# Kernel tuning notes

Hardware: AMD Instinct MI355X
Metric: run time of the kernel (lower is better)

## Reference

```python
import jax, jax.numpy as jnp
import numpy as np

B, N, D = 4096, 64, 128
H = 2
M = 3 * D            # model_dim = feat + edge + time
DK = M // H          # d_k = d_v = 192


def setup_inputs() -> dict:
    key = jax.random.key(0)
    ks = jax.random.split(key, 20)
    s = 0.02
    mask = jax.random.randint(ks[6], (B, N), 0, 2).astype(bool)
    mask = mask.at[:, 0].set(False)  # guarantee >=1 valid neighbor per row
    return {
        "src":   jax.random.normal(ks[0], (B, D), jnp.float32),
        "src_t": jax.random.normal(ks[1], (B, 1, D), jnp.float32),
        "src_s": jax.random.normal(ks[2], (B, D), jnp.float32),
        "seq":   jax.random.normal(ks[3], (B, N, D), jnp.float32),
        "seq_t": jax.random.normal(ks[4], (B, N, D), jnp.float32),
        "seq_e": jax.random.normal(ks[5], (B, N, D), jnp.float32),
        "mask":  mask,
        # MapBasedMultiHeadAttention params (torch Linear convention: [out, in])
        "Wq": jax.random.normal(ks[7], (M, M), jnp.float32) * s,
        "Wk": jax.random.normal(ks[8], (M, M), jnp.float32) * s,
        "Wv": jax.random.normal(ks[9], (M, M), jnp.float32) * s,
        "w_map": jax.random.normal(ks[10], (2 * DK,), jnp.float32) * s,
        "Wfc": jax.random.normal(ks[11], (M, M), jnp.float32) * s,
        "bfc": jnp.zeros((M,), jnp.float32),
        "ln_g": jnp.ones((M,), jnp.float32),
        "ln_b": jnp.zeros((M,), jnp.float32),
        # MergeLayer params
        "W1": jax.random.normal(ks[12], (D, M + D), jnp.float32) * s,
        "b1": jnp.zeros((D,), jnp.float32),
        "W2": jax.random.normal(ks[13], (D, D), jnp.float32) * s,
        "b2": jnp.zeros((D,), jnp.float32),
    }


def reference(src, src_t, src_s, seq, seq_t, seq_e, mask,
              Wq, Wk, Wv, w_map, Wfc, bfc, ln_g, ln_b, W1, b1, W2, b2):
    # AttnModel.forward with attn_mode='map', dropout in eval mode.
    q_in = jnp.concatenate([src[:, None, :], src_s[:, None, :], src_t], axis=2)  # [B,1,M]
    k_in = jnp.concatenate([seq, seq_e, seq_t], axis=2)                           # [B,N,M]

    qp = (q_in @ Wq.T).reshape(B, 1, H, DK)   # [B,1,H,dk]
    kp = (k_in @ Wk.T).reshape(B, N, H, DK)   # [B,N,H,dk]
    vp = (k_in @ Wv.T).reshape(B, N, H, DK)   # [B,N,H,dv]

    # weight_map(cat([q,k])) decomposes exactly: w1.q + w2.k (no bias, no nonlinearity before softmax)
    w1, w2 = w_map[:DK], w_map[DK:]
    logit = (jnp.einsum('bqhd,d->bhq', qp, w1)[:, :, :, None]
             + jnp.einsum('bnhd,d->bhn', kp, w2)[:, :, None, :])  # [B,H,1,N]
    logit = jnp.where(mask[:, None, None, :], -1e10, logit)
    attn = jax.nn.softmax(logit, axis=-1)                          # [B,H,1,N]

    out = jnp.einsum('bhqn,bnhd->bqhd', attn, vp).reshape(B, M)    # len_q == 1
    out = jax.nn.leaky_relu(out @ Wfc.T + bfc, negative_slope=0.2)
    out = out + q_in[:, 0, :]                                       # residual
    mu = out.mean(-1, keepdims=True)
    var = ((out - mu) ** 2).mean(-1, keepdims=True)
    out = (out - mu) / jnp.sqrt(var + 1e-5) * ln_g + ln_b           # LayerNorm

    # MergeLayer(output, src)
    x = jnp.concatenate([out, src], axis=1)                         # [B, M+D]
    h = jax.nn.relu(x @ W1.T + b1)
    output = h @ W2.T + b2                                          # [B, D]

    # torch attn after squeeze: [n_head*B, N], head-major
    attn_out = attn[:, :, 0, :].transpose(1, 0, 2).reshape(H * B, N)
    return output, attn_out
```

## Files before the change

### kernel.cpp

```cpp
#include <hip/hip_runtime.h>
#include <hip/hip_bf16.h>

#define B_ 4096
#define N_ 64
#define D_ 128
#define H_ 2
#define M_ 384
#define DK_ 192

#define WS_WKEFF 64
#define WS_W1T   1024
#define WS_W2T   66560
#define WS_WVB   82944
#define WS_WFCB  156672
#define WS_CTXB  230400
#define WS_R     2589696
#define WS_TOTAL 4162560

typedef __attribute__((ext_vector_type(8))) short bf16x8;
typedef __attribute__((ext_vector_type(4))) float f32x4;

__device__ __forceinline__ unsigned short bf1(float a) {
    return __builtin_bit_cast(unsigned short, __float2bfloat16(a));
}

__global__ __launch_bounds__(256) void prep2(
    const float* __restrict__ Wk, const float* __restrict__ wmap,
    const float* __restrict__ W1, const float* __restrict__ W2,
    const float* __restrict__ Wv, const float* __restrict__ Wfc,
    const void* __restrict__ mask, int* __restrict__ flag,
    float* __restrict__ wkeff, float* __restrict__ W1t, float* __restrict__ W2t,
    unsigned short* __restrict__ Wvb, unsigned short* __restrict__ Wfcb) {
    const int tid = threadIdx.x;
    if (blockIdx.x == 0 && tid == 0) {
        const unsigned int* u = (const unsigned int*)mask;
        bool all01 = true, allf = true;
        for (int i = 0; i < 64; ++i) {
            unsigned int v = u[i];
            if (v != 0u && v != 1u) all01 = false;
            if (v != 0u && v != 0x3f800000u) allf = false;
        }
        *flag = all01 ? 0 : (allf ? 2 : 1);
    }
    const int lane = tid & 63, wave = tid >> 6;
    const int gw = blockIdx.x * 4 + wave;
    if (gw < H_ * M_) {
        const int h = gw / M_, m = gw - h * M_;
        float s = 0.f;
        #pragma unroll
        for (int i = 0; i < 3; ++i) {
            int d = lane + i * 64;
            s += wmap[DK_ + d] * Wk[(size_t)(h * DK_ + d) * M_ + m];
        }
        #pragma unroll
        for (int off = 1; off < 64; off <<= 1) s += __shfl_xor(s, off, 64);
        if (lane == 0) wkeff[gw] = s;
    }
    const int gt = blockIdx.x * 256 + tid;
    const int stride = gridDim.x * 256;
    for (int i = gt; i < (M_ + D_) * D_; i += stride) {
        int k = i >> 7, o = i & 127;
        W1t[i] = W1[(size_t)o * (M_ + D_) + k];
    }
    for (int i = gt; i < D_ * D_; i += stride) {
        int k = i >> 7, o = i & 127;
        W2t[i] = W2[(size_t)o * D_ + k];
    }
    for (int i = gt; i < M_ * M_; i += stride) {
        Wvb[i]  = bf1(Wv[i]);
        Wfcb[i] = bf1(Wfc[i]);
    }
}

template <bool NT>
__device__ __forceinline__ float4 ld4(const float* p) {
    if (NT) {
        f32x4 r = __builtin_nontemporal_load((const f32x4*)p);
        return *(float4*)&r;
    }
    return *(const float4*)p;
}

template <bool NT>
__global__ __launch_bounds__(256) void attn_v4k(
    const float* __restrict__ seq, const float* __restrict__ seqE,
    const float* __restrict__ seqT, const void* __restrict__ mask,
    const float* __restrict__ wkeff, const int* __restrict__ flagp,
    unsigned short* __restrict__ ctxb, float* __restrict__ attn_out, int b0off) {
    __shared__ float scacc[4][16][50];
    __shared__ float swl[2][64];
    __shared__ float sel[4][2];

    const int b = blockIdx.x + b0off;
    const int tid = threadIdx.x;
    const int lane = tid & 63;
    const int wv = tid >> 6;
    const int j8 = tid & 15;
    const int g = tid >> 4;
    const int flag = *flagp;

    float wr0[24], wr1[24];
    #pragma unroll
    for (int t = 0; t < 3; ++t) {
        float4 a0 = *(const float4*)&wkeff[t * 128 + j8 * 8];
        float4 a1 = *(const float4*)&wkeff[t * 128 + j8 * 8 + 4];
        float4 b0 = *(const float4*)&wkeff[M_ + t * 128 + j8 * 8];
        float4 b1 = *(const float4*)&wkeff[M_ + t * 128 + j8 * 8 + 4];
        wr0[t*8+0]=a0.x; wr0[t*8+1]=a0.y; wr0[t*8+2]=a0.z; wr0[t*8+3]=a0.w;
        wr0[t*8+4]=a1.x; wr0[t*8+5]=a1.y; wr0[t*8+6]=a1.z; wr0[t*8+7]=a1.w;
        wr1[t*8+0]=b0.x; wr1[t*8+1]=b0.y; wr1[t*8+2]=b0.z; wr1[t*8+3]=b0.w;
        wr1[t*8+4]=b1.x; wr1[t*8+5]=b1.y; wr1[t*8+6]=b1.z; wr1[t*8+7]=b1.w;
    }

    float cacc0[24], cacc1[24];
    #pragma unroll
    for (int j = 0; j < 24; ++j) { cacc0[j] = 0.f; cacc1[j] = 0.f; }
    float el0 = 0.f, el1 = 0.f;

    const size_t bbase = (size_t)b * (N_ * D_);

    #pragma unroll
    for (int it = 0; it < 4; ++it) {
        const int n = g + (it << 4);
        const size_t off = bbase + (size_t)n * 128 + j8 * 8;
        float v[24];
        {
            float4 va0 = ld4<NT>(&seq [off]);
            float4 va1 = ld4<NT>(&seq [off + 4]);
            float4 vb0 = ld4<NT>(&seqE[off]);
            float4 vb1 = ld4<NT>(&seqE[off + 4]);
            float4 vc0 = ld4<NT>(&seqT[off]);
            float4 vc1 = ld4<NT>(&seqT[off + 4]);
            v[0]=va0.x; v[1]=va0.y; v[2]=va0.z; v[3]=va0.w;
            v[4]=va1.x; v[5]=va1.y; v[6]=va1.z; v[7]=va1.w;
            v[8]=vb0.x; v[9]=vb0.y; v[10]=vb0.z; v[11]=vb0.w;
            v[12]=vb1.x; v[13]=vb1.y; v[14]=vb1.z; v[15]=vb1.w;
            v[16]=vc0.x; v[17]=vc0.y; v[18]=vc0.z; v[19]=vc0.w;
            v[20]=vc1.x; v[21]=vc1.y; v[22]=vc1.z; v[23]=vc1.w;
        }
        float a0 = 0.f, a1 = 0.f;
        #pragma unroll
        for (int j = 0; j < 24; ++j) { a0 += v[j] * wr0[j]; a1 += v[j] * wr1[j]; }
        #pragma unroll
        for (int o = 1; o < 16; o <<= 1) {
            a0 += __shfl_xor(a0, o, 64);
            a1 += __shfl_xor(a1, o, 64);
        }
        int mv;
        if (flag == 0)      mv = ((const int*)mask)[(size_t)b * N_ + n];
        else if (flag == 1) mv = ((const unsigned char*)mask)[(size_t)b * N_ + n];
        else                mv = (((const unsigned int*)mask)[(size_t)b * N_ + n] != 0u) ? 1 : 0;
        float w0, w1;
        if (mv) { w0 = 0.f; w1 = 0.f; }
        else    { w0 = __expf(a0); w1 = __expf(a1); }
        el0 += w0; el1 += w1;
        if (j8 == 0) { swl[0][n] = w0; swl[1][n] = w1; }
        #pragma unroll
        for (int j = 0; j < 24; ++j) { cacc0[j] += w0 * v[j]; cacc1[j] += w1 * v[j]; }
    }

    #pragma unroll
    for (int o = 16; o <= 32; o <<= 1) {
        #pragma unroll
        for (int j = 0; j < 24; ++j) {
            cacc0[j] += __shfl_xor(cacc0[j], o, 64);
            cacc1[j] += __shfl_xor(cacc1[j], o, 64);
        }
    }
    #pragma unroll
    for (int o = 1; o < 64; o <<= 1) {
        el0 += __shfl_xor(el0, o, 64);
        el1 += __shfl_xor(el1, o, 64);
    }
    if (lane < 16) {
        float* dst = &scacc[wv][lane][0];
        #pragma unroll
        for (int j = 0; j < 24; ++j) { dst[j] = cacc0[j]; dst[24 + j] = cacc1[j]; }
    }
    if (lane == 0) { sel[wv][0] = el0; sel[wv][1] = el1; }
    __syncthreads();

    const float l0 = (sel[0][0] + sel[1][0] + sel[2][0] + sel[3][0]) * 0.0625f;
    const float l1 = (sel[0][1] + sel[1][1] + sel[2][1] + sel[3][1]) * 0.0625f;
    const float r0i = 1.f / l0, r1i = 1.f / l1;

    for (int o = tid; o < H_ * M_; o += 256) {
        const int h = (o >= M_) ? 1 : 0;
        const int m = o - h * M_;
        const int t = m >> 7, c = m & 127;
        const int jm = c >> 3, jj = c & 7;
        const int idx = h * 24 + t * 8 + jj;
        float s = scacc[0][jm][idx] + scacc[1][jm][idx] + scacc[2][jm][idx] + scacc[3][jm][idx];
        ctxb[(size_t)b * (H_ * M_) + o] = bf1(s * (h ? r1i : r0i));
    }
    if (tid < H_ * N_) {
        const int h = tid >> 6, n = tid & 63;
        attn_out[((size_t)h * B_ + b) * N_ + n] = swl[h][n] * (h ? r1i : r0i);
    }
}

#define SOUTSTRIDE 392
__global__ __launch_bounds__(256) void gemm_vfc(
    const unsigned short* __restrict__ ctxb, const unsigned short* __restrict__ Wvb,
    const unsigned short* __restrict__ Wfcb, const float* __restrict__ bfc,
    const float* __restrict__ src, const float* __restrict__ src_s, const float* __restrict__ src_t,
    float* __restrict__ rws) {
    __shared__ __hip_bfloat16 sout[16 * SOUTSTRIDE];
    const int tid = threadIdx.x;
    const int wave = tid >> 6, lane = tid & 63;
    const int r0 = blockIdx.x * 16;
    const int lr = lane & 15, lk = (lane >> 4) * 8;
    const int aOff = (wave >= 2) ? M_ : 0;

    f32x4 acc[6] = {};
    const unsigned short* arow = &ctxb[(size_t)(r0 + lr) * (H_ * M_) + aOff + lk];
    #pragma unroll
    for (int kk = 0; kk < M_; kk += 32) {
        bf16x8 af = *(const bf16x8*)&arow[kk];
        #pragma unroll
        for (int jt = 0; jt < 6; ++jt) {
            const int j0 = wave * 96 + jt * 16;
            bf16x8 bfr = *(const bf16x8*)&Wvb[(size_t)(j0 + lr) * M_ + kk + lk];
            acc[jt] = __builtin_amdgcn_mfma_f32_16x16x32_bf16(af, bfr, acc[jt], 0, 0, 0);
        }
    }
    #pragma unroll
    for (int jt = 0; jt < 6; ++jt)
        #pragma unroll
        for (int q = 0; q < 4; ++q) {
            const int row = (lane >> 4) * 4 + q;
            sout[row * SOUTSTRIDE + wave * 96 + jt * 16 + lr] =
                __float2bfloat16(acc[jt][q]);
        }
    __syncthreads();

    f32x4 acc2[6] = {};
    #pragma unroll
    for (int kk = 0; kk < M_; kk += 32) {
        bf16x8 af = *(const bf16x8*)&sout[lr * SOUTSTRIDE + kk + lk];
        #pragma unroll
        for (int jt = 0; jt < 6; ++jt) {
            const int j0 = wave * 96 + jt * 16;
            bf16x8 bfr = *(const bf16x8*)&Wfcb[(size_t)(j0 + lr) * M_ + kk + lk];
            acc2[jt] = __builtin_amdgcn_mfma_f32_16x16x32_bf16(af, bfr, acc2[jt], 0, 0, 0);
        }
    }
    #pragma unroll
    for (int jt = 0; jt < 6; ++jt) {
        const int j0 = wave * 96 + jt * 16;
        const float* qsrc = (j0 < D_) ? src : (j0 < 2 * D_) ? src_s : src_t;
        const int joff = j0 - ((j0 < D_) ? 0 : (j0 < 2 * D_) ? D_ : 2 * D_);
        #pragma unroll
        for (int q = 0; q < 4; ++q) {
            const int row = r0 + (lane >> 4) * 4 + q;
            const int jc = j0 + lr;
            float t = acc2[jt][q] + bfc[jc];
            t = t > 0.f ? t : 0.2f * t;
            t += qsrc[(size_t)row * D_ + joff + lr];
            rws[(size_t)row * M_ + jc] = t;
        }
    }
}

__global__ __launch_bounds__(256) void ln_mlp(
    const float* __restrict__ rin, const float* __restrict__ src,
    const float* __restrict__ g, const float* __restrict__ bta,
    const float* __restrict__ W1t, const float* __restrict__ b1,
    const float* __restrict__ W2t, const float* __restrict__ b2,
    float* __restrict__ outp) {
    __shared__ float sa[8 * 520];
    __shared__ float sh[8 * 132];
    const int b0 = blockIdx.x * 8;
    const int tid = threadIdx.x;
    const int row = tid >> 5, part = tid & 31;
    const size_t gr = (size_t)(b0 + row);
    {
        const float* rr = &rin[gr * M_];
        float4 v[3];
        float s = 0.f, sq = 0.f;
        #pragma unroll
        for (int i = 0; i < 3; ++i) {
            v[i] = *(const float4*)&rr[(part + i * 32) * 4];
            s  += v[i].x + v[i].y + v[i].z + v[i].w;
            sq += v[i].x * v[i].x + v[i].y * v[i].y + v[i].z * v[i].z + v[i].w * v[i].w;
        }
        #pragma unroll
        for (int off = 1; off < 32; off <<= 1) {
            s += __shfl_xor(s, off, 64); sq += __shfl_xor(sq, off, 64);
        }
        float mu = s * (1.f / 384.f);
        float rs = rsqrtf(sq * (1.f / 384.f) - mu * mu + 1e-5f);
        #pragma unroll
        for (int i = 0; i < 3; ++i) {
            int k = (part + i * 32) * 4;
            float4 g4 = *(const float4*)&g[k];
            float4 b4 = *(const float4*)&bta[k];
            float4 z;
            z.x = (v[i].x - mu) * rs * g4.x + b4.x;
            z.y = (v[i].y - mu) * rs * g4.y + b4.y;
            z.z = (v[i].z - mu) * rs * g4.z + b4.z;
            z.w = (v[i].w - mu) * rs * g4.w + b4.w;
            *(float4*)&sa[row * 520 + k] = z;
        }
        *(float4*)&sa[row * 520 + M_ + part * 4] = *(const float4*)&src[gr * D_ + part * 4];
    }
    __syncthreads();
    const int c4 = part * 4;
    float acc[4] = {};
    const float* ar = &sa[row * 520];
    #pragma unroll 4
    for (int k4 = 0; k4 < 128; ++k4) {
        float4 a4 = *(const float4*)&ar[k4 * 4];
        #pragma unroll
        for (int j = 0; j < 4; ++j) {
            int k = k4 * 4 + j;
            float a = (j == 0) ? a4.x : (j == 1) ? a4.y : (j == 2) ? a4.z : a4.w;
            float4 w = *(const float4*)&W1t[k * D_ + c4];
            acc[0] += a * w.x; acc[1] += a * w.y; acc[2] += a * w.z; acc[3] += a * w.w;
        }
    }
    {
        float4 bb = *(const float4*)&b1[c4];
        float4 hh;
        hh.x = fmaxf(acc[0] + bb.x, 0.f);
        hh.y = fmaxf(acc[1] + bb.y, 0.f);
        hh.z = fmaxf(acc[2] + bb.z, 0.f);
        hh.w = fmaxf(acc[3] + bb.w, 0.f);
        *(float4*)&sh[row * 132 + c4] = hh;
    }
    __syncthreads();
    float acc2[4] = {};
    const float* hr = &sh[row * 132];
    #pragma unroll 4
    for (int k4 = 0; k4 < 32; ++k4) {
        float4 a4 = *(const float4*)&hr[k4 * 4];
        #pragma unroll
        for (int j = 0; j < 4; ++j) {
            int k = k4 * 4 + j;
            float a = (j == 0) ? a4.x : (j == 1) ? a4.y : (j == 2) ? a4.z : a4.w;
            float4 w = *(const float4*)&W2t[k * D_ + c4];
            acc2[0] += a * w.x; acc2[1] += a * w.y; acc2[2] += a * w.z; acc2[3] += a * w.w;
        }
    }
    float4 bb2 = *(const float4*)&b2[c4];
    float4 oo = make_float4(acc2[0] + bb2.x, acc2[1] + bb2.y, acc2[2] + bb2.z, acc2[3] + bb2.w);
    *(float4*)&outp[gr * D_ + c4] = oo;
}

extern "C" void kernel_launch(void* const* d_in, const int* in_sizes, int n_in,
                              void* d_out, int out_size, void* d_ws, size_t ws_size,
                              hipStream_t stream) {
    (void)in_sizes; (void)n_in; (void)out_size;
    const float* src   = (const float*)d_in[0];
    const float* src_t = (const float*)d_in[1];
    const float* src_s = (const float*)d_in[2];
    const float* seq   = (const float*)d_in[3];
    const float* seq_t = (const float*)d_in[4];
    const float* seq_e = (const float*)d_in[5];
    const void*  mask  = d_in[6];
    const float* Wk    = (const float*)d_in[8];
    const float* Wv    = (const float*)d_in[9];
    const float* wmap  = (const float*)d_in[10];
    const float* Wfc   = (const float*)d_in[11];
    const float* bfc   = (const float*)d_in[12];
    const float* ln_g  = (const float*)d_in[13];
    const float* ln_b  = (const float*)d_in[14];
    const float* W1    = (const float*)d_in[15];
    const float* b1    = (const float*)d_in[16];
    const float* W2    = (const float*)d_in[17];
    const float* b2    = (const float*)d_in[18];

    if (ws_size < (size_t)WS_TOTAL * sizeof(float)) return;
    float* wsf   = (float*)d_ws;
    int*   flagp = (int*)d_ws;
    float* wkeff = wsf + WS_WKEFF;
    float* W1t   = wsf + WS_W1T;
    float* W2t   = wsf + WS_W2T;
    unsigned short* Wvb   = (unsigned short*)(wsf + WS_WVB);
    unsigned short* Wfcb  = (unsigned short*)(wsf + WS_WFCB);
    unsigned short* ctxb  = (unsigned short*)(wsf + WS_CTXB);
    float* rws   = wsf + WS_R;
    float* outp     = (float*)d_out;
    float* attn_out = outp + (size_t)B_ * D_;

    prep2<<<256, 256, 0, stream>>>(Wk, wmap, W1, W2, Wv, Wfc, mask, flagp,
                                   wkeff, W1t, W2t, Wvb, Wfcb);
    attn_v4k<true><<<B_ / 2, 256, 0, stream>>>(seq, seq_e, seq_t, mask, wkeff, flagp,
                                               ctxb, attn_out, 0);
    attn_v4k<false><<<B_ / 2, 256, 0, stream>>>(seq, seq_e, seq_t, mask, wkeff, flagp,
                                                ctxb, attn_out, B_ / 2);
    gemm_vfc<<<256, 256, 0, stream>>>(ctxb, Wvb, Wfcb, bfc, src, src_s, src_t, rws);
    ln_mlp<<<512, 256, 0, stream>>>(rws, src, ln_g, ln_b, W1t, b1, W2t, b2, outp);
}
```

Before: 154.1 us.

## Fuse V/FC GEMM with LayerNorm+MLP and drop nontemporal loads

Merges the bf16 MFMA V/FC GEMM kernel with the LayerNorm and merge-MLP kernel into one 512-thread kernel. The residual rows stay in shared memory instead of round-tripping through a global workspace, which also removes one launch. The attention kernel's nontemporal-load template is replaced by plain loads for both halves. In exchange, the fused kernel runs only 256 blocks for the MLP stage, where the old ln_mlp launched 512, and uses more shared memory per block.

```diff
diff --git a/kernel.cpp b/kernel.cpp
--- a/kernel.cpp
+++ b/kernel.cpp
@@ -14,8 +14,7 @@
 #define WS_WVB   82944
 #define WS_WFCB  156672
 #define WS_CTXB  230400
-#define WS_R     2589696
-#define WS_TOTAL 4162560
+#define WS_TOTAL 1017088
 
 typedef __attribute__((ext_vector_type(8))) short bf16x8;
 typedef __attribute__((ext_vector_type(4))) float f32x4;
@@ -72,17 +71,7 @@
     }
 }
 
-template <bool NT>
-__device__ __forceinline__ float4 ld4(const float* p) {
-    if (NT) {
-        f32x4 r = __builtin_nontemporal_load((const f32x4*)p);
-        return *(float4*)&r;
-    }
-    return *(const float4*)p;
-}
-
-template <bool NT>
-__global__ __launch_bounds__(256) void attn_v4k(
+__global__ __launch_bounds__(256) void attn_v4(
     const float* __restrict__ seq, const float* __restrict__ seqE,
     const float* __restrict__ seqT, const void* __restrict__ mask,
     const float* __restrict__ wkeff, const int* __restrict__ flagp,
@@ -125,12 +114,12 @@
         const size_t off = bbase + (size_t)n * 128 + j8 * 8;
         float v[24];
         {
-            float4 va0 = ld4<NT>(&seq [off]);
-            float4 va1 = ld4<NT>(&seq [off + 4]);
-            float4 vb0 = ld4<NT>(&seqE[off]);
-            float4 vb1 = ld4<NT>(&seqE[off + 4]);
-            float4 vc0 = ld4<NT>(&seqT[off]);
-            float4 vc1 = ld4<NT>(&seqT[off + 4]);
+            float4 va0 = *(const float4*)&seq [off];
+            float4 va1 = *(const float4*)&seq [off + 4];
+            float4 vb0 = *(const float4*)&seqE[off];
+            float4 vb1 = *(const float4*)&seqE[off + 4];
+            float4 vc0 = *(const float4*)&seqT[off];
+            float4 vc1 = *(const float4*)&seqT[off + 4];
             v[0]=va0.x; v[1]=va0.y; v[2]=va0.z; v[3]=va0.w;
             v[4]=va1.x; v[5]=va1.y; v[6]=va1.z; v[7]=va1.w;
             v[8]=vb0.x; v[9]=vb0.y; v[10]=vb0.z; v[11]=vb0.w;
@@ -200,87 +189,84 @@
 }
 
 #define SOUTSTRIDE 392
-__global__ __launch_bounds__(256) void gemm_vfc(
+__global__ __launch_bounds__(512) void gemm_vfc_ln(
     const unsigned short* __restrict__ ctxb, const unsigned short* __restrict__ Wvb,
     const unsigned short* __restrict__ Wfcb, const float* __restrict__ bfc,
     const float* __restrict__ src, const float* __restrict__ src_s, const float* __restrict__ src_t,
-    float* __restrict__ rws) {
+    const float* __restrict__ g, const float* __restrict__ bta,
+    const float* __restrict__ W1t, const float* __restrict__ b1,
+    const float* __restrict__ W2t, const float* __restrict__ b2,
+    float* __restrict__ outp) {
     __shared__ __hip_bfloat16 sout[16 * SOUTSTRIDE];
+    __shared__ float sa[16 * 520];
+    __shared__ float sh[16 * 132];
     const int tid = threadIdx.x;
     const int wave = tid >> 6, lane = tid & 63;
     const int r0 = blockIdx.x * 16;
     const int lr = lane & 15, lk = (lane >> 4) * 8;
-    const int aOff = (wave >= 2) ? M_ : 0;
-
-    f32x4 acc[6] = {};
+    const int aOff = (wave >= 4) ? M_ : 0;
+
+    f32x4 acc[3] = {};
     const unsigned short* arow = &ctxb[(size_t)(r0 + lr) * (H_ * M_) + aOff + lk];
     #pragma unroll
     for (int kk = 0; kk < M_; kk += 32) {
         bf16x8 af = *(const bf16x8*)&arow[kk];
         #pragma unroll
-        for (int jt = 0; jt < 6; ++jt) {
-            const int j0 = wave * 96 + jt * 16;
+        for (int jt = 0; jt < 3; ++jt) {
+            const int j0 = wave * 48 + jt * 16;
             bf16x8 bfr = *(const bf16x8*)&Wvb[(size_t)(j0 + lr) * M_ + kk + lk];
             acc[jt] = __builtin_amdgcn_mfma_f32_16x16x32_bf16(af, bfr, acc[jt], 0, 0, 0);
         }
     }
     #pragma unroll
-    for (int jt = 0; jt < 6; ++jt)
+    for (int jt = 0; jt < 3; ++jt)
         #pragma unroll
         for (int q = 0; q < 4; ++q) {
             const int row = (lane >> 4) * 4 + q;
-            sout[row * SOUTSTRIDE + wave * 96 + jt * 16 + lr] =
-                __float2bfloat16(acc[jt][q]);
-        }
-    __syncthreads();
-
-    f32x4 acc2[6] = {};
+            sout[row * SOUTSTRIDE + wave * 48 + jt * 16 + lr] = __float2bfloat16(acc[jt][q]);
+        }
+    __syncthreads();
+
+    f32x4 acc2[3] = {};
     #pragma unroll
     for (int kk = 0; kk < M_; kk += 32) {
         bf16x8 af = *(const bf16x8*)&sout[lr * SOUTSTRIDE + kk + lk];
         #pragma unroll
-        for (int jt = 0; jt < 6; ++jt) {
-            const int j0 = wave * 96 + jt * 16;
+        for (int jt = 0; jt < 3; ++jt) {
+            const int j0 = wave * 48 + jt * 16;
             bf16x8 bfr = *(const bf16x8*)&Wfcb[(size_t)(j0 + lr) * M_ + kk + lk];
             acc2[jt] = __builtin_amdgcn_mfma_f32_16x16x32_bf16(af, bfr, acc2[jt], 0, 0, 0);
         }
     }
     #pragma unroll
-    for (int jt = 0; jt < 6; ++jt) {
-        const int j0 = wave * 96 + jt * 16;
+    for (int jt = 0; jt < 3; ++jt) {
+        const int j0 = wave * 48 + jt * 16;
         const float* qsrc = (j0 < D_) ? src : (j0 < 2 * D_) ? src_s : src_t;
         const int joff = j0 - ((j0 < D_) ? 0 : (j0 < 2 * D_) ? D_ : 2 * D_);
         #pragma unroll
         for (int q = 0; q < 4; ++q) {
-            const int row = r0 + (lane >> 4) * 4 + q;
+            const int row = (lane >> 4) * 4 + q;
             const int jc = j0 + lr;
             float t = acc2[jt][q] + bfc[jc];
             t = t > 0.f ? t : 0.2f * t;
-            t += qsrc[(size_t)row * D_ + joff + lr];
-            rws[(size_t)row * M_ + jc] = t;
-        }
-    }
-}
-
-__global__ __launch_bounds__(256) void ln_mlp(
-    const float* __restrict__ rin, const float* __restrict__ src,
-    const float* __restrict__ g, const float* __restrict__ bta,
-    const float* __restrict__ W1t, const float* __restrict__ b1,
-    const float* __restrict__ W2t, const float* __restrict__ b2,
-    float* __restrict__ outp) {
-    __shared__ float sa[8 * 520];
-    __shared__ float sh[8 * 132];
-    const int b0 = blockIdx.x * 8;
-    const int tid = threadIdx.x;
+            t += qsrc[(size_t)(r0 + row) * D_ + joff + lr];
+            sa[row * 520 + jc] = t;
+        }
+    }
+    {
+        const int row2 = tid >> 5, part2 = tid & 31;
+        *(float4*)&sa[row2 * 520 + M_ + part2 * 4] =
+            *(const float4*)&src[(size_t)(r0 + row2) * D_ + part2 * 4];
+    }
+    __syncthreads();
+
     const int row = tid >> 5, part = tid & 31;
-    const size_t gr = (size_t)(b0 + row);
     {
-        const float* rr = &rin[gr * M_];
         float4 v[3];
         float s = 0.f, sq = 0.f;
         #pragma unroll
         for (int i = 0; i < 3; ++i) {
-            v[i] = *(const float4*)&rr[(part + i * 32) * 4];
+            v[i] = *(const float4*)&sa[row * 520 + (part + i * 32) * 4];
             s  += v[i].x + v[i].y + v[i].z + v[i].w;
             sq += v[i].x * v[i].x + v[i].y * v[i].y + v[i].z * v[i].z + v[i].w * v[i].w;
         }
@@ -302,11 +288,11 @@
             z.w = (v[i].w - mu) * rs * g4.w + b4.w;
             *(float4*)&sa[row * 520 + k] = z;
         }
-        *(float4*)&sa[row * 520 + M_ + part * 4] = *(const float4*)&src[gr * D_ + part * 4];
-    }
-    __syncthreads();
+    }
+    __syncthreads();
+
     const int c4 = part * 4;
-    float acc[4] = {};
+    float accm[4] = {};
     const float* ar = &sa[row * 520];
     #pragma unroll 4
     for (int k4 = 0; k4 < 128; ++k4) {
@@ -316,20 +302,21 @@
             int k = k4 * 4 + j;
             float a = (j == 0) ? a4.x : (j == 1) ? a4.y : (j == 2) ? a4.z : a4.w;
             float4 w = *(const float4*)&W1t[k * D_ + c4];
-            acc[0] += a * w.x; acc[1] += a * w.y; acc[2] += a * w.z; acc[3] += a * w.w;
+            accm[0] += a * w.x; accm[1] += a * w.y; accm[2] += a * w.z; accm[3] += a * w.w;
         }
     }
     {
         float4 bb = *(const float4*)&b1[c4];
         float4 hh;
-        hh.x = fmaxf(acc[0] + bb.x, 0.f);
-        hh.y = fmaxf(acc[1] + bb.y, 0.f);
-        hh.z = fmaxf(acc[2] + bb.z, 0.f);
-        hh.w = fmaxf(acc[3] + bb.w, 0.f);
+        hh.x = fmaxf(accm[0] + bb.x, 0.f);
+        hh.y = fmaxf(accm[1] + bb.y, 0.f);
+        hh.z = fmaxf(accm[2] + bb.z, 0.f);
+        hh.w = fmaxf(accm[3] + bb.w, 0.f);
         *(float4*)&sh[row * 132 + c4] = hh;
     }
     __syncthreads();
-    float acc2[4] = {};
+
+    float accm2[4] = {};
     const float* hr = &sh[row * 132];
     #pragma unroll 4
     for (int k4 = 0; k4 < 32; ++k4) {
@@ -339,12 +326,12 @@
             int k = k4 * 4 + j;
             float a = (j == 0) ? a4.x : (j == 1) ? a4.y : (j == 2) ? a4.z : a4.w;
             float4 w = *(const float4*)&W2t[k * D_ + c4];
-            acc2[0] += a * w.x; acc2[1] += a * w.y; acc2[2] += a * w.z; acc2[3] += a * w.w;
+            accm2[0] += a * w.x; accm2[1] += a * w.y; accm2[2] += a * w.z; accm2[3] += a * w.w;
         }
     }
     float4 bb2 = *(const float4*)&b2[c4];
-    float4 oo = make_float4(acc2[0] + bb2.x, acc2[1] + bb2.y, acc2[2] + bb2.z, acc2[3] + bb2.w);
-    *(float4*)&outp[gr * D_ + c4] = oo;
+    float4 oo = make_float4(accm2[0] + bb2.x, accm2[1] + bb2.y, accm2[2] + bb2.z, accm2[3] + bb2.w);
+    *(float4*)&outp[(size_t)(r0 + row) * D_ + c4] = oo;
 }
 
 extern "C" void kernel_launch(void* const* d_in, const int* in_sizes, int n_in,
@@ -379,16 +366,15 @@
     unsigned short* Wvb   = (unsigned short*)(wsf + WS_WVB);
     unsigned short* Wfcb  = (unsigned short*)(wsf + WS_WFCB);
     unsigned short* ctxb  = (unsigned short*)(wsf + WS_CTXB);
-    float* rws   = wsf + WS_R;
     float* outp     = (float*)d_out;
     float* attn_out = outp + (size_t)B_ * D_;
 
     prep2<<<256, 256, 0, stream>>>(Wk, wmap, W1, W2, Wv, Wfc, mask, flagp,
                                    wkeff, W1t, W2t, Wvb, Wfcb);
-    attn_v4k<true><<<B_ / 2, 256, 0, stream>>>(seq, seq_e, seq_t, mask, wkeff, flagp,
-                                               ctxb, attn_out, 0);
-    attn_v4k<false><<<B_ / 2, 256, 0, stream>>>(seq, seq_e, seq_t, mask, wkeff, flagp,
-                                                ctxb, attn_out, B_ / 2);
-    gemm_vfc<<<256, 256, 0, stream>>>(ctxb, Wvb, Wfcb, bfc, src, src_s, src_t, rws);
-    ln_mlp<<<512, 256, 0, stream>>>(rws, src, ln_g, ln_b, W1t, b1, W2t, b2, outp);
-}
+    attn_v4<<<B_ / 2, 256, 0, stream>>>(seq, seq_e, seq_t, mask, wkeff, flagp,
+                                        ctxb, attn_out, 0);
+    attn_v4<<<B_ / 2, 256, 0, stream>>>(seq, seq_e, seq_t, mask, wkeff, flagp,
+                                        ctxb, attn_out, B_ / 2);
+    gemm_vfc_ln<<<256, 512, 0, stream>>>(ctxb, Wvb, Wfcb, bfc, src, src_s, src_t,
+                                         ln_g, ln_b, W1t, b1, W2t, b2, outp);
+}
```

New measurement: 162.9 us. +5.7%, slower.
